# Kernel optimization log

Hardware: AMD Instinct MI355X
Metric: run time of the kernel (lower is better)

The kernel has to match this reference:

```python
import jax, jax.numpy as jnp
import numpy as np

EPS = 1e-5          # module's self.eps
CLAMP = 1e-8        # numerical floor for norms
MAX_EUCLID = 32.0   # rescale_to_max_euclid cap (best-effort reconstruction)


def _linner(u, v):
    # Lorentz inner product <u,v>_L = -u0*v0 + <u_s,v_s>, keepdims on last axis
    uv = jnp.sum(u * v, axis=-1, keepdims=True)
    return uv - 2.0 * u[..., :1] * v[..., :1]


def _centroid(x):
    # Lorentzian (weighted) centroid: mean then renormalize onto hyperboloid (k=1)
    avg = jnp.mean(x, axis=-2)
    denom = jnp.sqrt(jnp.clip(-_linner(avg, avg), CLAMP, None))
    return avg / denom


def _logmap(x, y):
    # log_x(y) on Lorentz model, k=1
    alpha = jnp.clip(-_linner(x, y), 1.0 + 1e-7, None)
    u = y - alpha * x
    unorm = jnp.sqrt(jnp.clip(_linner(u, u), CLAMP, None))
    return jnp.arccosh(alpha) * u / unorm


def _plus_origin(y):
    # y + o where o = (1, 0, ..., 0)
    return jnp.concatenate([y[..., :1] + 1.0, y[..., 1:]], axis=-1)


def _transp0back(y, v):
    # parallel transport T_{y->o}(v): v + <o,v>_L/(1 - <y,o>_L) * (y + o); <o,v>_L = -v0
    coef = -v[..., :1] / (1.0 + y[..., :1])
    return v + coef * _plus_origin(y)


def _transp0(y, v):
    # parallel transport T_{o->y}(v): v + <y,v>_L/(1 + y0) * (o + y)
    coef = _linner(y, v) / (1.0 + y[..., :1])
    return v + coef * _plus_origin(y)


def _expmap(x, u):
    # exp_x(u) on Lorentz model, k=1
    nu = jnp.sqrt(jnp.clip(_linner(u, u), CLAMP, None))
    return jnp.cosh(nu) * x + jnp.sinh(nu) * u / nu


def _rescale_to_max_euclid(x):
    n = jnp.sqrt(jnp.sum(x * x, axis=-1, keepdims=True))
    return x * jnp.minimum(1.0, MAX_EUCLID / jnp.maximum(n, CLAMP))


def setup_inputs() -> dict:
    key = jax.random.key(0)
    B, S, D = 64, 4096, 128
    raw = 0.5 * jax.random.normal(key, (B, S, D - 1), dtype=jnp.float32)
    time = jnp.sqrt(1.0 + jnp.sum(raw * raw, axis=-1, keepdims=True))
    x = jnp.concatenate([time, raw], axis=-1)  # points on the hyperboloid
    gamma = jnp.ones((D,), dtype=jnp.float32)
    beta = jnp.zeros((D,), dtype=jnp.float32).at[0].set(1.0)  # manifold origin
    return {"x": x, "gamma": gamma, "beta": beta}


def reference(x, gamma, beta):
    # Training-mode Lorentz batchnorm (3D input path)
    mean = _centroid(x)       # (B, D)
    mean = _centroid(mean)    # (D,)
    x_T = _logmap(mean, x)            # tangent vectors at mean, (B, S, D)
    x_T = _transp0back(mean, x_T)     # transport to tangent space at origin
    var = jnp.sqrt(jnp.var(x_T, axis=(0, 1)) + EPS)   # Frechet per-feature std, (D,)
    x_T = x_T * (gamma / (var + EPS))
    x_T = _rescale_to_max_euclid(x_T)
    x_T = _transp0(beta, x_T)         # transport to tangent space at beta
    return _expmap(beta, x_T)
```

## Files before the change

### kernel.cpp

```cpp
#include <hip/hip_runtime.h>
#include <math.h>

#define NB 64
#define NS 4096
#define ND 128
#define NPTS (NB * NS)
#define PPB1 128
#define NBLK1 (NPTS / PPB1)
#define CHUNKS1 (NS / PPB1)
#define PPB 256
#define NBLK (NPTS / PPB)
#define EPSV 1e-5f
#define CLAMPV 1e-8f
#define MAXEUC 32.0f

typedef float nfloat4 __attribute__((ext_vector_type(4)));
typedef float nfloat2 __attribute__((ext_vector_type(2)));

__device__ __forceinline__ float4 nt_load4(const float4* p) {
    nfloat4 v = __builtin_nontemporal_load((const nfloat4*)p);
    return make_float4(v.x, v.y, v.z, v.w);
}
__device__ __forceinline__ float2 nt_load2(const float2* p) {
    nfloat2 v = __builtin_nontemporal_load((const nfloat2*)p);
    return make_float2(v.x, v.y);
}
__device__ __forceinline__ void nt_store4(const float4& v, float4* p) {
    nfloat4 nv = {v.x, v.y, v.z, v.w};
    __builtin_nontemporal_store(nv, (nfloat4*)p);
}

__device__ __forceinline__ float rcp_f(float x) { return __builtin_amdgcn_rcpf(x); }

#define DPP_ADD(v, ctrl)                                                            \
    v += __int_as_float(__builtin_amdgcn_update_dpp(0, __float_as_int(v), (ctrl),   \
                                                    0xF, 0xF, true))

__device__ __forceinline__ float row16_sum(float v) {
    DPP_ADD(v, 0x128);
    DPP_ADD(v, 0x124);
    DPP_ADD(v, 0x122);
    DPP_ADD(v, 0x121);
    return v;
}

__device__ __forceinline__ void point_scalars16(const float4& xa, const float4& xb,
                                                const float4& wa, const float4& wb,
                                                float inv1pm0, int fl,
                                                float& fac, float& hcoef) {
    float ad = wa.x * xa.x + wa.y * xa.y + wa.z * xa.z + wa.w * xa.w
             + wb.x * xb.x + wb.y * xb.y + wb.z * xb.z + wb.w * xb.w;
    float px = (fl == 0) ? xa.x : 0.f;
    ad = row16_sum(ad);
    px = row16_sum(px);
    float alpha = fmaxf(ad, 1.0f + 1e-7f);
    float am1 = alpha * alpha - 1.f;
    float sq = sqrtf(fmaxf(am1, CLAMPV));
    fac = __logf(alpha + sq) * rcp_f(sq);
    hcoef = -fac * (alpha + px) * inv1pm0;
}

__global__ __launch_bounds__(256, 8) void k1(const float4* __restrict__ x4,
                                             float4* __restrict__ part1_4) {
    const int tid = threadIdx.x;
    const long long base = (long long)blockIdx.x * (PPB1 * 32);
    float4 acc = make_float4(0.f, 0.f, 0.f, 0.f);
#pragma unroll 8
    for (int i = 0; i < PPB1 * 32 / 256; ++i) {
        float4 v = x4[base + i * 256 + tid];
        acc.x += v.x; acc.y += v.y; acc.z += v.z; acc.w += v.w;
    }
    __shared__ float4 ls4[8][32];
    ls4[tid >> 5][tid & 31] = acc;
    __syncthreads();
    if (tid < 32) {
        float4 s = ls4[0][tid];
#pragma unroll
        for (int c = 1; c < 8; ++c) {
            float4 v = ls4[c][tid];
            s.x += v.x; s.y += v.y; s.z += v.z; s.w += v.w;
        }
        part1_4[blockIdx.x * 32 + tid] = s;
    }
}

__global__ __launch_bounds__(1024) void k2(const float* __restrict__ part1,
                                           float* __restrict__ meanG) {
    __shared__ float avgL[NB][ND];
    const int w = threadIdx.x >> 6, l = threadIdx.x & 63;
    for (int b = w; b < NB; b += 16) {
        float a0 = 0.f, a1 = 0.f;
#pragma unroll
        for (int c = 0; c < CHUNKS1; ++c) {
            a0 += part1[(b * CHUNKS1 + c) * ND + l];
            a1 += part1[(b * CHUNKS1 + c) * ND + 64 + l];
        }
        a0 *= (1.0f / (float)NS);
        a1 *= (1.0f / (float)NS);
        float s = a0 * a0 + a1 * a1;
#pragma unroll
        for (int o = 32; o > 0; o >>= 1) s += __shfl_xor(s, o, 64);
        float a00 = __shfl(a0, 0, 64);
        float denom = sqrtf(fmaxf(2.f * a00 * a00 - s, CLAMPV));
        avgL[b][l] = a0 / denom;
        avgL[b][64 + l] = a1 / denom;
    }
    __syncthreads();
    if (w == 0) {
        float a0 = 0.f, a1 = 0.f;
        for (int b = 0; b < NB; ++b) { a0 += avgL[b][l]; a1 += avgL[b][64 + l]; }
        a0 *= (1.0f / (float)NB);
        a1 *= (1.0f / (float)NB);
        float s = a0 * a0 + a1 * a1;
#pragma unroll
        for (int o = 32; o > 0; o >>= 1) s += __shfl_xor(s, o, 64);
        float a00 = __shfl(a0, 0, 64);
        float denom = sqrtf(fmaxf(2.f * a00 * a00 - s, CLAMPV));
        meanG[l] = a0 / denom;
        meanG[64 + l] = a1 / denom;
    }
}

__global__ __launch_bounds__(256, 4) void k3(const float4* __restrict__ x4,
                                             const float* __restrict__ meanG,
                                             float* __restrict__ p3S,
                                             float* __restrict__ p3Q,
                                             float2* __restrict__ fchG) {
    const int fl = threadIdx.x & 15;
    const int pg = threadIdx.x >> 4;
    const float4* m4 = (const float4*)meanG;
    const float4 ma = m4[fl], mb = m4[fl + 16];
    const float m0 = meanG[0];
    const float inv1pm0 = rcp_f(1.f + m0);
    float4 wa = make_float4(-ma.x, -ma.y, -ma.z, -ma.w);
    float4 wb = make_float4(-mb.x, -mb.y, -mb.z, -mb.w);
    if (fl == 0) wa.x = ma.x;
    float4 sa = make_float4(0.f, 0.f, 0.f, 0.f), sb = sa, qa = sa, qb = sa;
    const long long base = (long long)blockIdx.x * PPB;
#pragma unroll 4
    for (int i = 0; i < PPB / 16; ++i) {
        long long p = base + i * 16 + pg;
        float4 xa = x4[p * 32 + fl];
        float4 xb = x4[p * 32 + fl + 16];
        float fac, hc;
        point_scalars16(xa, xb, wa, wb, inv1pm0, fl, fac, hc);
        if (fl == 0) fchG[p] = make_float2(fac, hc);
        float t0 = fac * xa.x + hc * ma.x;
        float t1 = fac * xa.y + hc * ma.y;
        float t2 = fac * xa.z + hc * ma.z;
        float t3 = fac * xa.w + hc * ma.w;
        float t4 = fac * xb.x + hc * mb.x;
        float t5 = fac * xb.y + hc * mb.y;
        float t6 = fac * xb.z + hc * mb.z;
        float t7 = fac * xb.w + hc * mb.w;
        if (fl == 0) t0 = 0.f;
        sa.x += t0; sa.y += t1; sa.z += t2; sa.w += t3;
        sb.x += t4; sb.y += t5; sb.z += t6; sb.w += t7;
        qa.x += t0 * t0; qa.y += t1 * t1; qa.z += t2 * t2; qa.w += t3 * t3;
        qb.x += t4 * t4; qb.y += t5 * t5; qb.z += t6 * t6; qb.w += t7 * t7;
    }
    __shared__ float ls[16][ND];
    __shared__ float lq[16][ND];
    float* ps = &ls[pg][fl * 8];
    float* pq = &lq[pg][fl * 8];
    ps[0] = sa.x; ps[1] = sa.y; ps[2] = sa.z; ps[3] = sa.w;
    ps[4] = sb.x; ps[5] = sb.y; ps[6] = sb.z; ps[7] = sb.w;
    pq[0] = qa.x; pq[1] = qa.y; pq[2] = qa.z; pq[3] = qa.w;
    pq[4] = qb.x; pq[5] = qb.y; pq[6] = qb.z; pq[7] = qb.w;
    __syncthreads();
    if (threadIdx.x < ND) {
        int d = threadIdx.x;
        int slot = ((d & 63) >> 2) * 8 + (d >> 6) * 4 + (d & 3);
        float S = 0.f, Q = 0.f;
#pragma unroll
        for (int cc = 0; cc < 16; ++cc) { S += ls[cc][slot]; Q += lq[cc][slot]; }
        p3S[d * NBLK + blockIdx.x] = S;
        p3Q[d * NBLK + blockIdx.x] = Q;
    }
}

__global__ __launch_bounds__(256) void k4(const float* __restrict__ p3S,
                                          const float* __restrict__ p3Q,
                                          const float* __restrict__ gamma,
                                          float* __restrict__ scaleG) {
    const int d = blockIdx.x;
    const int t = threadIdx.x;
    const float4* vS = (const float4*)(p3S + d * NBLK);
    const float4* vQ = (const float4*)(p3Q + d * NBLK);
    float4 a = vS[t];
    float4 b = vQ[t];
    __shared__ double dredS[256];
    __shared__ double dredQ[256];
    dredS[t] = (double)a.x + (double)a.y + (double)a.z + (double)a.w;
    dredQ[t] = (double)b.x + (double)b.y + (double)b.z + (double)b.w;
    __syncthreads();
    for (int o = 128; o > 0; o >>= 1) {
        if (t < o) { dredS[t] += dredS[t + o]; dredQ[t] += dredQ[t + o]; }
        __syncthreads();
    }
    if (t == 0) {
        const double N = (double)NPTS;
        double mu = dredS[0] / N;
        double var = dredQ[0] / N - mu * mu;
        if (var < 0.0) var = 0.0;
        float stdv = sqrtf((float)var + EPSV);
        scaleG[d] = gamma[d] / (stdv + EPSV);
    }
}

__global__ __launch_bounds__(256, 4) void k5(const float4* __restrict__ x4,
                                             const float* __restrict__ meanG,
                                             const float* __restrict__ scaleG,
                                             const float* __restrict__ betaG,
                                             const float2* __restrict__ fchG,
                                             float4* __restrict__ out4) {
    const int fl = threadIdx.x & 15;
    const int pg = threadIdx.x >> 4;
    const float4* m4 = (const float4*)meanG;
    const float4* s4 = (const float4*)scaleG;
    const float4* b4 = (const float4*)betaG;
    const float4 ma = m4[fl], mb = m4[fl + 16];
    const float4 sca = s4[fl], scb = s4[fl + 16];
    const float4 bta = b4[fl], btb = b4[fl + 16];
    const float b0 = betaG[0];
    const float inv1pb0 = rcp_f(1.f + b0);
    const long long base = (long long)blockIdx.x * PPB;
#pragma unroll 4
    for (int i = 0; i < PPB / 16; ++i) {
        long long p = base + i * 16 + pg;
        float4 xa = nt_load4(&x4[p * 32 + fl]);
        float4 xb = nt_load4(&x4[p * 32 + fl + 16]);
        float2 fh = nt_load2(&fchG[p]);
        float fac = fh.x, hc = fh.y;
        float ts0 = sca.x * (fac * xa.x + hc * ma.x);
        float ts1 = sca.y * (fac * xa.y + hc * ma.y);
        float ts2 = sca.z * (fac * xa.z + hc * ma.z);
        float ts3 = sca.w * (fac * xa.w + hc * ma.w);
        float ts4 = scb.x * (fac * xb.x + hc * mb.x);
        float ts5 = scb.y * (fac * xb.y + hc * mb.y);
        float ts6 = scb.z * (fac * xb.z + hc * mb.z);
        float ts7 = scb.w * (fac * xb.w + hc * mb.w);
        if (fl == 0) ts0 = 0.f;
        float nn = ts0 * ts0 + ts1 * ts1 + ts2 * ts2 + ts3 * ts3
                 + ts4 * ts4 + ts5 * ts5 + ts6 * ts6 + ts7 * ts7;
        float bd = bta.x * ts0 + bta.y * ts1 + bta.z * ts2 + bta.w * ts3
                 + btb.x * ts4 + btb.y * ts5 + btb.z * ts6 + btb.w * ts7;
        nn = row16_sum(nn);
        bd = row16_sum(bd);
        float n = sqrtf(nn);
        float r = fminf(1.f, MAXEUC * rcp_f(fmaxf(n, CLAMPV)));
        float coef2 = r * bd * inv1pb0;
        float nu = fmaxf(r * n, 1e-4f);
        float e = __expf(nu);
        float ei = rcp_f(e);
        float ch = 0.5f * (e + ei);
        float sf = (0.5f * (e - ei)) * rcp_f(nu);
        float A = ch + sf * coef2;
        float Bc = sf * r;
        float4 oa, ob;
        oa.x = Bc * ts0 + A * bta.x;
        oa.y = Bc * ts1 + A * bta.y;
        oa.z = Bc * ts2 + A * bta.z;
        oa.w = Bc * ts3 + A * bta.w;
        ob.x = Bc * ts4 + A * btb.x;
        ob.y = Bc * ts5 + A * btb.y;
        ob.z = Bc * ts6 + A * btb.z;
        ob.w = Bc * ts7 + A * btb.w;
        if (fl == 0) oa.x += sf * coef2;
        nt_store4(oa, &out4[p * 32 + fl]);
        nt_store4(ob, &out4[p * 32 + fl + 16]);
    }
}

extern "C" void kernel_launch(void* const* d_in, const int* in_sizes, int n_in,
                              void* d_out, int out_size, void* d_ws, size_t ws_size,
                              hipStream_t stream) {
    const float* x = (const float*)d_in[0];
    const float* gamma = (const float*)d_in[1];
    const float* beta = (const float*)d_in[2];
    float* out = (float*)d_out;
    float* ws = (float*)d_ws;

    float* part1  = ws;
    float* meanG  = part1 + NBLK1 * ND;
    float* scaleG = meanG + ND;
    float* p3S    = scaleG + ND;
    float* p3Q    = p3S + ND * NBLK;
    float2* fchG  = (float2*)(p3Q + ND * NBLK);

    k1<<<NBLK1, 256, 0, stream>>>((const float4*)x, (float4*)part1);
    k2<<<1, 1024, 0, stream>>>(part1, meanG);
    k3<<<NBLK, 256, 0, stream>>>((const float4*)x, meanG, p3S, p3Q, fchG);
    k4<<<ND, 256, 0, stream>>>(p3S, p3Q, gamma, scaleG);
    k5<<<NBLK, 256, 0, stream>>>((const float4*)x, meanG, scaleG, beta, fchG,
                                 (float4*)out);
}
```

Measured before the change: 294.4 us.

## Halve points per block and software-prefetch next iteration loads in k3/k5

Points per block in the statistics and output kernels drop from 256 to 128, doubling the grid. Both loops are fully unrolled with explicit register double-buffering, so the next point's x and scalars are loaded while the current point is computed. The k5 loads switch from nontemporal to ordinary cached loads so that x can hit in the cache after k3 has read it. k4 is adjusted to read two float4 per thread to cover the doubled partial-sum count, at the cost of more partials to reduce and higher register pressure.

New measurement: 295.1 us. About the same (+0.2%).

```diff
diff --git a/kernel.cpp b/kernel.cpp
--- a/kernel.cpp
+++ b/kernel.cpp
@@ -8,23 +8,15 @@
 #define PPB1 128
 #define NBLK1 (NPTS / PPB1)
 #define CHUNKS1 (NS / PPB1)
-#define PPB 256
+#define PPB 128
 #define NBLK (NPTS / PPB)
+#define ITERS (PPB / 16)
 #define EPSV 1e-5f
 #define CLAMPV 1e-8f
 #define MAXEUC 32.0f
 
 typedef float nfloat4 __attribute__((ext_vector_type(4)));
-typedef float nfloat2 __attribute__((ext_vector_type(2)));
-
-__device__ __forceinline__ float4 nt_load4(const float4* p) {
-    nfloat4 v = __builtin_nontemporal_load((const nfloat4*)p);
-    return make_float4(v.x, v.y, v.z, v.w);
-}
-__device__ __forceinline__ float2 nt_load2(const float2* p) {
-    nfloat2 v = __builtin_nontemporal_load((const nfloat2*)p);
-    return make_float2(v.x, v.y);
-}
+
 __device__ __forceinline__ void nt_store4(const float4& v, float4* p) {
     nfloat4 nv = {v.x, v.y, v.z, v.w};
     __builtin_nontemporal_store(nv, (nfloat4*)p);
@@ -137,11 +129,17 @@
     if (fl == 0) wa.x = ma.x;
     float4 sa = make_float4(0.f, 0.f, 0.f, 0.f), sb = sa, qa = sa, qb = sa;
     const long long base = (long long)blockIdx.x * PPB;
-#pragma unroll 4
-    for (int i = 0; i < PPB / 16; ++i) {
+    float4 xa = x4[(base + pg) * 32 + fl];
+    float4 xb = x4[(base + pg) * 32 + fl + 16];
+#pragma unroll
+    for (int i = 0; i < ITERS; ++i) {
+        float4 na, nb;
+        if (i + 1 < ITERS) {
+            long long pn = base + (i + 1) * 16 + pg;
+            na = x4[pn * 32 + fl];
+            nb = x4[pn * 32 + fl + 16];
+        }
         long long p = base + i * 16 + pg;
-        float4 xa = x4[p * 32 + fl];
-        float4 xb = x4[p * 32 + fl + 16];
         float fac, hc;
         point_scalars16(xa, xb, wa, wb, inv1pm0, fl, fac, hc);
         if (fl == 0) fchG[p] = make_float2(fac, hc);
@@ -158,6 +156,7 @@
         sb.x += t4; sb.y += t5; sb.z += t6; sb.w += t7;
         qa.x += t0 * t0; qa.y += t1 * t1; qa.z += t2 * t2; qa.w += t3 * t3;
         qb.x += t4 * t4; qb.y += t5 * t5; qb.z += t6 * t6; qb.w += t7 * t7;
+        xa = na; xb = nb;
     }
     __shared__ float ls[16][ND];
     __shared__ float lq[16][ND];
@@ -187,12 +186,14 @@
     const int t = threadIdx.x;
     const float4* vS = (const float4*)(p3S + d * NBLK);
     const float4* vQ = (const float4*)(p3Q + d * NBLK);
-    float4 a = vS[t];
-    float4 b = vQ[t];
+    float4 a0 = vS[t], a1 = vS[t + 256];
+    float4 b0 = vQ[t], b1 = vQ[t + 256];
     __shared__ double dredS[256];
     __shared__ double dredQ[256];
-    dredS[t] = (double)a.x + (double)a.y + (double)a.z + (double)a.w;
-    dredQ[t] = (double)b.x + (double)b.y + (double)b.z + (double)b.w;
+    dredS[t] = (double)a0.x + (double)a0.y + (double)a0.z + (double)a0.w
+             + (double)a1.x + (double)a1.y + (double)a1.z + (double)a1.w;
+    dredQ[t] = (double)b0.x + (double)b0.y + (double)b0.z + (double)b0.w
+             + (double)b1.x + (double)b1.y + (double)b1.z + (double)b1.w;
     __syncthreads();
     for (int o = 128; o > 0; o >>= 1) {
         if (t < o) { dredS[t] += dredS[t + o]; dredQ[t] += dredQ[t + o]; }
@@ -225,12 +226,19 @@
     const float b0 = betaG[0];
     const float inv1pb0 = rcp_f(1.f + b0);
     const long long base = (long long)blockIdx.x * PPB;
-#pragma unroll 4
-    for (int i = 0; i < PPB / 16; ++i) {
+    float4 xa = x4[(base + pg) * 32 + fl];
+    float4 xb = x4[(base + pg) * 32 + fl + 16];
+    float2 fh = fchG[base + pg];
+#pragma unroll
+    for (int i = 0; i < ITERS; ++i) {
+        float4 na, nb; float2 nf;
+        if (i + 1 < ITERS) {
+            long long pn = base + (i + 1) * 16 + pg;
+            na = x4[pn * 32 + fl];
+            nb = x4[pn * 32 + fl + 16];
+            nf = fchG[pn];
+        }
         long long p = base + i * 16 + pg;
-        float4 xa = nt_load4(&x4[p * 32 + fl]);
-        float4 xb = nt_load4(&x4[p * 32 + fl + 16]);
-        float2 fh = nt_load2(&fchG[p]);
         float fac = fh.x, hc = fh.y;
         float ts0 = sca.x * (fac * xa.x + hc * ma.x);
         float ts1 = sca.y * (fac * xa.y + hc * ma.y);
@@ -269,6 +277,7 @@
         if (fl == 0) oa.x += sf * coef2;
         nt_store4(oa, &out4[p * 32 + fl]);
         nt_store4(ob, &out4[p * 32 + fl + 16]);
+        xa = na; xb = nb; fh = nf;
     }
 }
 
```
